# Kernel tuning notes

Hardware: AMD Instinct MI355X
Metric: run time of the kernel (lower is better)

## Reference

```python
import jax, jax.numpy as jnp
import numpy as np

B, T, D, H = 512, 1024, 64, 128

def setup_inputs() -> dict:
    key = jax.random.key(0)
    ks = jax.random.split(key, 9)
    s_ih = 1.0 / np.sqrt(H)
    inp = {
        "x_seq": jax.random.normal(ks[0], (B, T, D), dtype=jnp.float32),
        # PyTorch LSTM params, gate order (i, f, g, o)
        "W_ih": jax.random.uniform(ks[1], (4 * H, D), minval=-s_ih, maxval=s_ih, dtype=jnp.float32),
        "W_hh": jax.random.uniform(ks[2], (4 * H, H), minval=-s_ih, maxval=s_ih, dtype=jnp.float32),
        "b_ih": jax.random.uniform(ks[3], (4 * H,), minval=-s_ih, maxval=s_ih, dtype=jnp.float32),
        "b_hh": jax.random.uniform(ks[4], (4 * H,), minval=-s_ih, maxval=s_ih, dtype=jnp.float32),
        # fc head: Linear(H,64) -> ReLU -> Linear(64,1)
        "W1": jax.random.uniform(ks[5], (64, H), minval=-s_ih, maxval=s_ih, dtype=jnp.float32),
        "b1": jax.random.uniform(ks[6], (64,), minval=-s_ih, maxval=s_ih, dtype=jnp.float32),
        "W2": jax.random.uniform(ks[7], (1, 64), minval=-0.125, maxval=0.125, dtype=jnp.float32),
        "b2": jax.random.uniform(ks[8], (1,), minval=-0.125, maxval=0.125, dtype=jnp.float32),
    }
    return inp


def _lstm_last(x_seq, W_ih, W_hh, b_ih, b_hh):
    # Precompute input projections for all timesteps in one big GEMM: [T,B,4H]
    xg = jnp.einsum('btd,gd->tbg', x_seq, W_ih) + b_ih + b_hh
    h0 = jnp.zeros((x_seq.shape[0], W_hh.shape[1]), dtype=x_seq.dtype)
    c0 = jnp.zeros_like(h0)
    Hd = W_hh.shape[1]

    def step(carry, xg_t):
        h, c = carry
        gates = xg_t + h @ W_hh.T  # [B,4H], gate order i,f,g,o
        i = jax.nn.sigmoid(gates[:, 0 * Hd:1 * Hd])
        f = jax.nn.sigmoid(gates[:, 1 * Hd:2 * Hd])
        g = jnp.tanh(gates[:, 2 * Hd:3 * Hd])
        o = jax.nn.sigmoid(gates[:, 3 * Hd:4 * Hd])
        c_new = f * c + i * g
        h_new = o * jnp.tanh(c_new)
        return (h_new, c_new), None

    (h_last, _), _ = jax.lax.scan(step, (h0, c0), xg)
    return h_last  # [B,H] == out[:, -1, :]


def reference(x_seq, W_ih, W_hh, b_ih, b_hh, W1, b1, W2, b2):
    h_last = _lstm_last(x_seq, W_ih, W_hh, b_ih, b_hh)
    z = jax.nn.relu(h_last @ W1.T + b1)
    y = z @ W2.T + b2  # [B,1]
    return y[:, 0]
```

## Files before the change

kernel.cpp:

```cpp
#include <hip/hip_runtime.h>


#define BB 512
#define TT 1024
#define DD 64
#define HH 128
#define GG 512

typedef _Float16 half2_t __attribute__((ext_vector_type(2)));

__device__ __forceinline__ float dot2(half2_t a, half2_t b, float c) {
#if __has_builtin(__builtin_amdgcn_fdot2)
    return __builtin_amdgcn_fdot2(a, b, c, false);
#else
    return c + (float)a[0] * (float)b[0] + (float)a[1] * (float)b[1];
#endif
}

__device__ __forceinline__ half2_t pack2(float a, float b) {
    half2_t r;
    r[0] = (_Float16)a;
    r[1] = (_Float16)b;
    return r;
}

__device__ __forceinline__ half2_t bc(unsigned int u) {
    return __builtin_bit_cast(half2_t, u);
}

__device__ __forceinline__ float sigm(float x) {
    return 1.f / (1.f + __expf(-x));
}
__device__ __forceinline__ float tanh_f(float x) {
    return 1.f - 2.f / (__expf(2.f * x) + 1.f);
}

__global__ __launch_bounds__(512, 1)
void lstm_fused_kernel(const float* __restrict__ x_seq,
                       const float* __restrict__ W_ih,
                       const float* __restrict__ W_hh,
                       const float* __restrict__ b_ih,
                       const float* __restrict__ b_hh,
                       const float* __restrict__ W1v,
                       const float* __restrict__ b1v,
                       const float* __restrict__ W2v,
                       const float* __restrict__ b2v,
                       float* __restrict__ out)
{
    const int tid = threadIdx.x;
    const int b0  = blockIdx.x * 2;

    __shared__ __align__(16) _Float16 xs[2][2][DD];
    __shared__ __align__(16) _Float16 hs[2][HH];
    __shared__ __align__(16) float    gl[2][GG];

    half2_t wih[32];
    half2_t whh[64];
#pragma unroll
    for (int k = 0; k < 16; ++k) {
        const float4 w = reinterpret_cast<const float4*>(W_ih + tid * DD)[k];
        wih[2 * k]     = pack2(w.x, w.y);
        wih[2 * k + 1] = pack2(w.z, w.w);
    }
#pragma unroll
    for (int k = 0; k < 32; ++k) {
        const float4 w = reinterpret_cast<const float4*>(W_hh + tid * HH)[k];
        whh[2 * k]     = pack2(w.x, w.y);
        whh[2 * k + 1] = pack2(w.z, w.w);
    }
    const float bias = b_ih[tid] + b_hh[tid];

    if (tid < 256) hs[tid >> 7][tid & 127] = (_Float16)0.f;
    if (tid < 128) {
        const int r = tid >> 6, k = tid & 63;
        xs[0][r][k] = (_Float16)x_seq[((b0 + r) * TT + 0) * DD + k];
    }
    float c_reg = 0.f;
    __syncthreads();

    const int pr = tid >> 6, pk = tid & 63;

    for (int t = 0; t < TT; ++t) {
        const int cur = t & 1;

        float xpre = 0.f;
        const bool do_pre = (t + 1 < TT) && (tid < 128);
        if (do_pre) xpre = x_seq[((b0 + pr) * TT + (t + 1)) * DD + pk];

        const uint4* h0 = reinterpret_cast<const uint4*>(hs[0]);
        const uint4* h1 = reinterpret_cast<const uint4*>(hs[1]);
        const uint4* x0 = reinterpret_cast<const uint4*>(xs[cur][0]);
        const uint4* x1 = reinterpret_cast<const uint4*>(xs[cur][1]);

        float a0 = bias, b0a = 0.f;
        float a1 = bias, b1a = 0.f;
#pragma unroll
        for (int k = 0; k < 16; ++k) {
            const uint4 v0 = h0[k];
            const uint4 v1 = h1[k];
            a0  = dot2(whh[4 * k + 0], bc(v0.x), a0);
            a1  = dot2(whh[4 * k + 0], bc(v1.x), a1);
            b0a = dot2(whh[4 * k + 1], bc(v0.y), b0a);
            b1a = dot2(whh[4 * k + 1], bc(v1.y), b1a);
            a0  = dot2(whh[4 * k + 2], bc(v0.z), a0);
            a1  = dot2(whh[4 * k + 2], bc(v1.z), a1);
            b0a = dot2(whh[4 * k + 3], bc(v0.w), b0a);
            b1a = dot2(whh[4 * k + 3], bc(v1.w), b1a);
        }
#pragma unroll
        for (int k = 0; k < 8; ++k) {
            const uint4 v0 = x0[k];
            const uint4 v1 = x1[k];
            a0  = dot2(wih[4 * k + 0], bc(v0.x), a0);
            a1  = dot2(wih[4 * k + 0], bc(v1.x), a1);
            b0a = dot2(wih[4 * k + 1], bc(v0.y), b0a);
            b1a = dot2(wih[4 * k + 1], bc(v1.y), b1a);
            a0  = dot2(wih[4 * k + 2], bc(v0.z), a0);
            a1  = dot2(wih[4 * k + 2], bc(v1.z), a1);
            b0a = dot2(wih[4 * k + 3], bc(v0.w), b0a);
            b1a = dot2(wih[4 * k + 3], bc(v1.w), b1a);
        }
        gl[0][tid] = a0 + b0a;
        gl[1][tid] = a1 + b1a;

        if (do_pre) xs[cur ^ 1][pr][pk] = (_Float16)xpre;
        __syncthreads();

        if (tid < 256) {
            const int r = tid >> 7, u = tid & 127;
            const float gi = gl[r][u];
            const float gf = gl[r][HH + u];
            const float gg = gl[r][2 * HH + u];
            const float go = gl[r][3 * HH + u];
            c_reg = sigm(gf) * c_reg + sigm(gi) * tanh_f(gg);
            hs[r][u] = (_Float16)(sigm(go) * tanh_f(c_reg));
        }
        __syncthreads();
    }

    if (tid < 128) {
        const int r = tid >> 6, j = tid & 63;
        float z = b1v[j];
        const float* w1 = W1v + j * HH;
#pragma unroll 16
        for (int k = 0; k < HH; ++k)
            z = fmaf(w1[k], (float)hs[r][k], z);
        z = fmaxf(z, 0.f) * W2v[j];
#pragma unroll
        for (int off = 32; off; off >>= 1)
            z += __shfl_down(z, off, 64);
        if (j == 0) out[b0 + r] = z + b2v[0];
    }
}

extern "C" void kernel_launch(void* const* d_in, const int* in_sizes, int n_in,
                              void* d_out, int out_size, void* d_ws, size_t ws_size,
                              hipStream_t stream) {
    const float* x_seq = (const float*)d_in[0];
    const float* W_ih  = (const float*)d_in[1];
    const float* W_hh  = (const float*)d_in[2];
    const float* b_ih  = (const float*)d_in[3];
    const float* b_hh  = (const float*)d_in[4];
    const float* W1    = (const float*)d_in[5];
    const float* b1    = (const float*)d_in[6];
    const float* W2    = (const float*)d_in[7];
    const float* b2    = (const float*)d_in[8];
    float* out = (float*)d_out;

    lstm_fused_kernel<<<BB / 2, 512, 0, stream>>>(
        x_seq, W_ih, W_hh, b_ih, b_hh, W1, b1, W2, b2, out);
}
```

Measured before the change: 1.332 ms.

## Split gate dot products over 4 threads with 1024-thread blocks

Each block now uses 1024 threads. Every gate row's 192-long concatenated [h,x] dot product is split across 4 lanes of 48 elements, then combined with xor shuffles, and each thread handles two gate rows for two batch rows. h and x share a double-buffered fused shared array, and the x prefetch moves to the top warps so it overlaps the gate-update threads. The aim is to shorten the per-timestep serial dot chain and lower per-thread register pressure. The cost is shuffle reductions, more threads contending at each barrier, and a hand-written inline-asm v_dot2 instruction.

```diff
diff --git a/kernel.cpp b/kernel.cpp
--- a/kernel.cpp
+++ b/kernel.cpp
@@ -5,16 +5,13 @@
 #define TT 1024
 #define DD 64
 #define HH 128
-#define GG 512
+#define KK 192
 
 typedef _Float16 half2_t __attribute__((ext_vector_type(2)));
 
 __device__ __forceinline__ float dot2(half2_t a, half2_t b, float c) {
-#if __has_builtin(__builtin_amdgcn_fdot2)
-    return __builtin_amdgcn_fdot2(a, b, c, false);
-#else
-    return c + (float)a[0] * (float)b[0] + (float)a[1] * (float)b[1];
-#endif
+    asm("v_dot2_f32_f16 %0, %1, %2, %0" : "+v"(c) : "v"(a), "v"(b));
+    return c;
 }
 
 __device__ __forceinline__ half2_t pack2(float a, float b) {
@@ -35,7 +32,14 @@
     return 1.f - 2.f / (__expf(2.f * x) + 1.f);
 }
 
-__global__ __launch_bounds__(512, 1)
+__device__ __forceinline__ half2_t wld(const float* __restrict__ Whh,
+                                       const float* __restrict__ Wih,
+                                       int gate, int k) {
+    if (k < HH) return pack2(Whh[gate * HH + k], Whh[gate * HH + k + 1]);
+    return pack2(Wih[gate * DD + (k - HH)], Wih[gate * DD + (k - HH) + 1]);
+}
+
+__global__ __launch_bounds__(1024, 4)
 void lstm_fused_kernel(const float* __restrict__ x_seq,
                        const float* __restrict__ W_ih,
                        const float* __restrict__ W_hh,
@@ -48,93 +52,87 @@
                        float* __restrict__ out)
 {
     const int tid = threadIdx.x;
+    const int q   = tid & 3;
+    const int g   = tid >> 2;
     const int b0  = blockIdx.x * 2;
 
-    __shared__ __align__(16) _Float16 xs[2][2][DD];
-    __shared__ __align__(16) _Float16 hs[2][HH];
-    __shared__ __align__(16) float    gl[2][GG];
+    __shared__ __align__(16) _Float16 hx[2][2][KK];
+    __shared__ __align__(16) float    gl[2][4 * HH];
 
-    half2_t wih[32];
-    half2_t whh[64];
+    const int k0 = q * 48;
+    half2_t wa[24], wb[24];
 #pragma unroll
-    for (int k = 0; k < 16; ++k) {
-        const float4 w = reinterpret_cast<const float4*>(W_ih + tid * DD)[k];
-        wih[2 * k]     = pack2(w.x, w.y);
-        wih[2 * k + 1] = pack2(w.z, w.w);
+    for (int j = 0; j < 24; ++j) {
+        wa[j] = wld(W_hh, W_ih, g,       k0 + 2 * j);
+        wb[j] = wld(W_hh, W_ih, g + 256, k0 + 2 * j);
     }
-#pragma unroll
-    for (int k = 0; k < 32; ++k) {
-        const float4 w = reinterpret_cast<const float4*>(W_hh + tid * HH)[k];
-        whh[2 * k]     = pack2(w.x, w.y);
-        whh[2 * k + 1] = pack2(w.z, w.w);
-    }
-    const float bias = b_ih[tid] + b_hh[tid];
+    const float biasA = b_ih[g] + b_hh[g];
+    const float biasB = b_ih[g + 256] + b_hh[g + 256];
 
-    if (tid < 256) hs[tid >> 7][tid & 127] = (_Float16)0.f;
+    if (tid < 256) hx[0][tid >> 7][tid & 127] = (_Float16)0.f;
     if (tid < 128) {
         const int r = tid >> 6, k = tid & 63;
-        xs[0][r][k] = (_Float16)x_seq[((b0 + r) * TT + 0) * DD + k];
+        hx[0][r][HH + k] = (_Float16)x_seq[((b0 + r) * TT + 0) * DD + k];
     }
     float c_reg = 0.f;
+    const int pr = (tid - 896) >> 6;
+    const int pk = (tid - 896) & 63;
     __syncthreads();
-
-    const int pr = tid >> 6, pk = tid & 63;
 
     for (int t = 0; t < TT; ++t) {
         const int cur = t & 1;
 
         float xpre = 0.f;
-        const bool do_pre = (t + 1 < TT) && (tid < 128);
+        const bool do_pre = (t + 1 < TT) && (tid >= 896);
         if (do_pre) xpre = x_seq[((b0 + pr) * TT + (t + 1)) * DD + pk];
 
-        const uint4* h0 = reinterpret_cast<const uint4*>(hs[0]);
-        const uint4* h1 = reinterpret_cast<const uint4*>(hs[1]);
-        const uint4* x0 = reinterpret_cast<const uint4*>(xs[cur][0]);
-        const uint4* x1 = reinterpret_cast<const uint4*>(xs[cur][1]);
+        const uint4* s0 = reinterpret_cast<const uint4*>(&hx[cur][0][k0]);
+        const uint4* s1 = reinterpret_cast<const uint4*>(&hx[cur][1][k0]);
+        float aA0 = 0.f, aA1 = 0.f, aB0 = 0.f, aB1 = 0.f;
+#pragma unroll
+        for (int j = 0; j < 6; ++j) {
+            const uint4 v0 = s0[j];
+            const uint4 v1 = s1[j];
+            aA0 = dot2(wa[4 * j + 0], bc(v0.x), aA0);
+            aA1 = dot2(wa[4 * j + 0], bc(v1.x), aA1);
+            aB0 = dot2(wb[4 * j + 0], bc(v0.x), aB0);
+            aB1 = dot2(wb[4 * j + 0], bc(v1.x), aB1);
+            aA0 = dot2(wa[4 * j + 1], bc(v0.y), aA0);
+            aA1 = dot2(wa[4 * j + 1], bc(v1.y), aA1);
+            aB0 = dot2(wb[4 * j + 1], bc(v0.y), aB0);
+            aB1 = dot2(wb[4 * j + 1], bc(v1.y), aB1);
+            aA0 = dot2(wa[4 * j + 2], bc(v0.z), aA0);
+            aA1 = dot2(wa[4 * j + 2], bc(v1.z), aA1);
+            aB0 = dot2(wb[4 * j + 2], bc(v0.z), aB0);
+            aB1 = dot2(wb[4 * j + 2], bc(v1.z), aB1);
+            aA0 = dot2(wa[4 * j + 3], bc(v0.w), aA0);
+            aA1 = dot2(wa[4 * j + 3], bc(v1.w), aA1);
+            aB0 = dot2(wb[4 * j + 3], bc(v0.w), aB0);
+            aB1 = dot2(wb[4 * j + 3], bc(v1.w), aB1);
+        }
 
-        float a0 = bias, b0a = 0.f;
-        float a1 = bias, b1a = 0.f;
-#pragma unroll
-        for (int k = 0; k < 16; ++k) {
-            const uint4 v0 = h0[k];
-            const uint4 v1 = h1[k];
-            a0  = dot2(whh[4 * k + 0], bc(v0.x), a0);
-            a1  = dot2(whh[4 * k + 0], bc(v1.x), a1);
-            b0a = dot2(whh[4 * k + 1], bc(v0.y), b0a);
-            b1a = dot2(whh[4 * k + 1], bc(v1.y), b1a);
-            a0  = dot2(whh[4 * k + 2], bc(v0.z), a0);
-            a1  = dot2(whh[4 * k + 2], bc(v1.z), a1);
-            b0a = dot2(whh[4 * k + 3], bc(v0.w), b0a);
-            b1a = dot2(whh[4 * k + 3], bc(v1.w), b1a);
-        }
-#pragma unroll
-        for (int k = 0; k < 8; ++k) {
-            const uint4 v0 = x0[k];
-            const uint4 v1 = x1[k];
-            a0  = dot2(wih[4 * k + 0], bc(v0.x), a0);
-            a1  = dot2(wih[4 * k + 0], bc(v1.x), a1);
-            b0a = dot2(wih[4 * k + 1], bc(v0.y), b0a);
-            b1a = dot2(wih[4 * k + 1], bc(v1.y), b1a);
-            a0  = dot2(wih[4 * k + 2], bc(v0.z), a0);
-            a1  = dot2(wih[4 * k + 2], bc(v1.z), a1);
-            b0a = dot2(wih[4 * k + 3], bc(v0.w), b0a);
-            b1a = dot2(wih[4 * k + 3], bc(v1.w), b1a);
-        }
-        gl[0][tid] = a0 + b0a;
-        gl[1][tid] = a1 + b1a;
+        aA0 += __shfl_xor(aA0, 1, 64); aA0 += __shfl_xor(aA0, 2, 64);
+        aA1 += __shfl_xor(aA1, 1, 64); aA1 += __shfl_xor(aA1, 2, 64);
+        aB0 += __shfl_xor(aB0, 1, 64); aB0 += __shfl_xor(aB0, 2, 64);
+        aB1 += __shfl_xor(aB1, 1, 64); aB1 += __shfl_xor(aB1, 2, 64);
 
-        if (do_pre) xs[cur ^ 1][pr][pk] = (_Float16)xpre;
+        const float v  = (q == 0) ? aA0 : (q == 1) ? aA1 : (q == 2) ? aB0 : aB1;
+        const float bb = (q < 2) ? biasA : biasB;
+        const int   row = q & 1;
+        const int   gg  = (q < 2) ? g : g + 256;
+        gl[row][gg] = v + bb;
         __syncthreads();
 
         if (tid < 256) {
             const int r = tid >> 7, u = tid & 127;
             const float gi = gl[r][u];
             const float gf = gl[r][HH + u];
-            const float gg = gl[r][2 * HH + u];
+            const float gG = gl[r][2 * HH + u];
             const float go = gl[r][3 * HH + u];
-            c_reg = sigm(gf) * c_reg + sigm(gi) * tanh_f(gg);
-            hs[r][u] = (_Float16)(sigm(go) * tanh_f(c_reg));
+            c_reg = sigm(gf) * c_reg + sigm(gi) * tanh_f(gG);
+            hx[cur ^ 1][r][u] = (_Float16)(sigm(go) * tanh_f(c_reg));
         }
+        if (do_pre) hx[cur ^ 1][pr][HH + pk] = (_Float16)xpre;
         __syncthreads();
     }
 
@@ -144,7 +142,7 @@
         const float* w1 = W1v + j * HH;
 #pragma unroll 16
         for (int k = 0; k < HH; ++k)
-            z = fmaf(w1[k], (float)hs[r][k], z);
+            z = fmaf(w1[k], (float)hx[0][r][k], z);
         z = fmaxf(z, 0.f) * W2v[j];
 #pragma unroll
         for (int off = 32; off; off >>= 1)
@@ -167,6 +165,6 @@
     const float* b2    = (const float*)d_in[8];
     float* out = (float*)d_out;
 
-    lstm_fused_kernel<<<BB / 2, 512, 0, stream>>>(
+    lstm_fused_kernel<<<BB / 2, 1024, 0, stream>>>(
         x_seq, W_ih, W_hh, b_ih, b_hh, W1, b1, W2, b2, out);
 }
```

After: 1.487 ms. +11.6%, slower.
